# Kernel optimization log

Measured on AMD Instinct MI355X. Metric: run time of the kernel, lower is better.

Reference implementation:

```python
import jax, jax.numpy as jnp
import numpy as np

# ---- problem dims ----
B, S, C, H, W = 4, 8, 3, 256, 256
P = 68          # keypoints (self.points)
DS = 4          # detector downsample
WIN = 8
STEPS = 10      # Gauss-Newton iterations per frame pair
EPS = 1e-6
GRAY_W = jnp.array([0.299, 0.587, 0.114], dtype=jnp.float32)

# window offsets [K,2] in (x,y)
_rng = jnp.arange(-WIN, WIN + 1, dtype=jnp.float32)
_OFF = jnp.stack(jnp.meshgrid(_rng, _rng, indexing='xy'), -1).reshape(-1, 2)


def setup_inputs() -> dict:
    key = jax.random.key(0)
    k1, k2 = jax.random.split(key)
    inputs = jax.random.normal(k1, (B, S, C, H, W), dtype=jnp.float32)
    Wdet = jax.random.normal(k2, (P, C, 3, 3), dtype=jnp.float32) * 0.1
    bdet = jnp.zeros((P,), dtype=jnp.float32)
    return {"inputs": inputs, "Wdet": Wdet, "bdet": bdet}


def _bilinear(img, xy):
    # img [H,W]; xy [...,2] in (x,y) pixel coords -> sampled values [...]
    x = jnp.clip(xy[..., 0], 0.0, W - 1.001)
    y = jnp.clip(xy[..., 1], 0.0, H - 1.001)
    x0 = jnp.floor(x); y0 = jnp.floor(y)
    wx = x - x0; wy = y - y0
    x0i = x0.astype(jnp.int32); y0i = y0.astype(jnp.int32)
    x1i = jnp.minimum(x0i + 1, W - 1); y1i = jnp.minimum(y0i + 1, H - 1)
    v00 = img[y0i, x0i]; v01 = img[y0i, x1i]
    v10 = img[y1i, x0i]; v11 = img[y1i, x1i]
    return (1 - wy) * ((1 - wx) * v00 + wx * v01) + wy * ((1 - wx) * v10 + wx * v11)


def _grad_xy(img):
    # central differences with edge replication
    px = jnp.pad(img, ((0, 0), (1, 1)), mode='edge')
    py = jnp.pad(img, ((1, 1), (0, 0)), mode='edge')
    gx = (px[:, 2:] - px[:, :-2]) * 0.5
    gy = (py[2:, :] - py[:-2, :]) * 0.5
    return gx, gy


def _lk_track(old, new, pts):
    # one Lucas-Kanade tracking step: old/new [H,W] gray, pts [P,2] -> [P,2]
    gx, gy = _grad_xy(old)
    pos0 = pts[:, None, :] + _OFF[None]            # [P,K,2]
    I0 = _bilinear(old, pos0)                      # [P,K] template patch
    Ix = _bilinear(gx, pos0)
    Iy = _bilinear(gy, pos0)
    Gxx = (Ix * Ix).sum(-1); Gxy = (Ix * Iy).sum(-1); Gyy = (Iy * Iy).sum(-1)
    det = Gxx * Gyy - Gxy * Gxy + EPS
    Ginv = jnp.stack([jnp.stack([Gyy, -Gxy], -1),
                      jnp.stack([-Gxy, Gxx], -1)], -2) / det[:, None, None]  # [P,2,2]

    def step(i, v):
        I1 = _bilinear(new, pos0 + v[:, None, :])  # [P,K]
        err = I0 - I1
        b = jnp.stack([(err * Ix).sum(-1), (err * Iy).sum(-1)], -1)  # [P,2]
        return v + jnp.einsum('pij,pj->pi', Ginv, b)

    v = jax.lax.fori_loop(0, STEPS, step, jnp.zeros_like(pts))
    return pts + v


def _lk_forward_backward(gray, locs):
    # gray [S,H,W], locs [S,P,2] -> nextPts, fbackPts, backPts each [S,P,2]
    def f(pts, frames):
        o, n = frames
        q = _lk_track(o, n, pts)
        return q, q

    # forward: track detector locs of frame 0 through the sequence
    _, fout = jax.lax.scan(f, locs[0], (gray[:-1], gray[1:]))
    nextPts = jnp.concatenate([locs[:1], fout], 0)
    ro, rn = gray[1:][::-1], gray[:-1][::-1]
    # forward-backward: track the forward end point back to frame 0
    _, fbout = jax.lax.scan(f, nextPts[-1], (ro, rn))
    fbackPts = jnp.concatenate([nextPts[-1:], fbout], 0)[::-1]
    # backward: track detector locs of last frame back through the sequence
    _, bout = jax.lax.scan(f, locs[-1], (ro, rn))
    backPts = jnp.concatenate([locs[-1:], bout], 0)[::-1]
    return nextPts, fbackPts, backPts


def _detector(x, Wdet, bdet):
    # x [N,C,H,W] -> heatmaps [N,P,H/DS,W/DS], locs [N,P,2] (pixel coords), scores [N,P]
    hm = jax.lax.conv_general_dilated(
        x, Wdet, window_strides=(DS, DS), padding='SAME',
        dimension_numbers=('NCHW', 'OIHW', 'NCHW')) + bdet[None, :, None, None]
    N, _, Hd, Wd = hm.shape
    flat = hm.reshape(N, P, Hd * Wd)
    prob = jax.nn.softmax(flat, axis=-1)
    ys, xs = jnp.meshgrid(jnp.arange(Hd, dtype=hm.dtype),
                          jnp.arange(Wd, dtype=hm.dtype), indexing='ij')
    ex = (prob * xs.reshape(-1)).sum(-1) * DS   # soft-argmax, upscaled to input px
    ey = (prob * ys.reshape(-1)).sum(-1) * DS
    locs = jnp.stack([ex, ey], -1)
    scos = flat.max(-1)
    return hm, locs, scos


def reference(inputs, Wdet, bdet):
    x = inputs.reshape(B * S, C, H, W)
    hm, locs, scos = _detector(x, Wdet, bdet)
    heatmaps = hm.reshape(B, S, P, H // DS, W // DS)
    batch_locs = locs.reshape(B, S, P, 2)
    batch_scos = scos.reshape(B, S, P)
    gray = jnp.einsum('bschw,c->bshw', inputs, GRAY_W)  # [B,S,H,W]
    nextPts, fbackPts, backPts = jax.vmap(_lk_forward_backward)(gray, batch_locs)
    return heatmaps, batch_locs, batch_scos, nextPts, fbackPts, backPts
```

## Files before the change

kernel.cpp:

```cpp
#include <hip/hip_runtime.h>
#include <math.h>

namespace {
constexpr int Bn = 4, Sn = 8, Cn = 3, Himg = 256, Wimg = 256;
constexpr int Pn = 68, DS = 4, WIN = 8, STEPS = 10;
constexpr int HWi = Himg * Wimg;
constexpr int NIMG = Bn * Sn;
constexpr int HD = Himg / DS, WD = Wimg / DS;
constexpr int Kwin = (2 * WIN + 1) * (2 * WIN + 1);
constexpr int P2ROWS = 257;
constexpr int P2FR = P2ROWS * 256;
constexpr int NSHIFT = NIMG * P2FR;
}

__global__ __launch_bounds__(256) void conv_kernel(const float* __restrict__ x,
                                                   const float* __restrict__ Wdet,
                                                   const float* __restrict__ bdet,
                                                   float* __restrict__ hm) {
    __shared__ float wsh[Pn * 27];
    __shared__ float bsh[Pn];
    __shared__ float insh[3][3][Wimg];
    int n = blockIdx.x >> 6;
    int oy = blockIdx.x & 63;
    int tid = threadIdx.x;
    for (int t = tid; t < Pn * 27; t += 256) wsh[t] = Wdet[t];
    if (tid < Pn) bsh[tid] = bdet[tid];
    for (int t = tid; t < 3 * 3 * Wimg; t += 256) {
        int c = t / (3 * Wimg);
        int r = (t / Wimg) % 3;
        int col = t % Wimg;
        insh[c][r][col] = x[(size_t)n * 3 * HWi + (size_t)c * HWi + (oy * 4 + r) * Wimg + col];
    }
    __syncthreads();
    int ox = tid & 63;
    int wid = tid >> 6;
    float in_reg[27];
    #pragma unroll
    for (int c = 0; c < 3; c++)
        #pragma unroll
        for (int ky = 0; ky < 3; ky++)
            #pragma unroll
            for (int kx = 0; kx < 3; kx++)
                in_reg[c * 9 + ky * 3 + kx] = insh[c][ky][ox * 4 + kx];
    #pragma unroll
    for (int i = 0; i < 17; i++) {
        int p = wid + i * 4;
        const float* w = &wsh[p * 27];
        float acc = bsh[p];
        #pragma unroll
        for (int j = 0; j < 27; j++) acc += w[j] * in_reg[j];
        hm[(size_t)n * Pn * 4096 + (size_t)p * 4096 + oy * 64 + ox] = acc;
    }
}

__global__ __launch_bounds__(256) void smax_kernel(const float* __restrict__ hm,
                                                   float* __restrict__ locs,
                                                   float* __restrict__ scos) {
    int row = blockIdx.x;
    const float4* r = (const float4*)(hm + (size_t)row * 4096);
    int tid = threadIdx.x;
    float v[16];
    #pragma unroll
    for (int j = 0; j < 4; j++) {
        float4 q = r[tid + 256 * j];
        v[4 * j + 0] = q.x; v[4 * j + 1] = q.y; v[4 * j + 2] = q.z; v[4 * j + 3] = q.w;
    }
    float m = v[0];
    #pragma unroll
    for (int i = 1; i < 16; i++) m = fmaxf(m, v[i]);
    __shared__ float redm[4];
    #pragma unroll
    for (int o = 32; o; o >>= 1) m = fmaxf(m, __shfl_xor(m, o, 64));
    int wid = tid >> 6, lane = tid & 63;
    if (lane == 0) redm[wid] = m;
    __syncthreads();
    m = fmaxf(fmaxf(redm[0], redm[1]), fmaxf(redm[2], redm[3]));
    float s = 0.f, sx = 0.f, sy = 0.f;
    #pragma unroll
    for (int j = 0; j < 4; j++) {
        #pragma unroll
        for (int q = 0; q < 4; q++) {
            int e = (tid + 256 * j) * 4 + q;
            float ev = expf(v[4 * j + q] - m);
            s += ev;
            sx += ev * (float)(e & 63);
            sy += ev * (float)(e >> 6);
        }
    }
    #pragma unroll
    for (int o = 32; o; o >>= 1) {
        s  += __shfl_xor(s, o, 64);
        sx += __shfl_xor(sx, o, 64);
        sy += __shfl_xor(sy, o, 64);
    }
    __shared__ float reds[3][4];
    if (lane == 0) { reds[0][wid] = s; reds[1][wid] = sx; reds[2][wid] = sy; }
    __syncthreads();
    if (tid == 0) {
        float S_ = reds[0][0] + reds[0][1] + reds[0][2] + reds[0][3];
        float SX = reds[1][0] + reds[1][1] + reds[1][2] + reds[1][3];
        float SY = reds[2][0] + reds[2][1] + reds[2][2] + reds[2][3];
        locs[(size_t)row * 2 + 0] = SX / S_ * 4.0f;
        locs[(size_t)row * 2 + 1] = SY / S_ * 4.0f;
        scos[row] = m;
    }
}

__global__ __launch_bounds__(256) void grayP2_kernel(const float* __restrict__ in,
                                                     float2* __restrict__ P2r,
                                                     float2* __restrict__ P2rs) {
    __shared__ float g[9][257];
    int blk = blockIdx.x;
    int n = blk / 33, q = blk % 33;
    int tid = threadIdx.x;
    const float* base = in + (size_t)n * 3 * HWi;
    #pragma unroll
    for (int r = 0; r < 9; r++) {
        int row = min(max(8 * q - 1 + r, 0), 255);
        int a = row * Wimg + tid;
        g[r][tid] = 0.299f * base[a] + 0.587f * base[a + HWi] + 0.114f * base[a + 2 * HWi];
    }
    if (tid < 9) g[tid][256] = g[tid][255];
    __syncthreads();
    float2* pr = P2r + (size_t)n * P2FR;
    float2* ps = P2rs + (size_t)n * P2FR;
    #pragma unroll
    for (int j = 0; j < 8; j++) {
        int k = 8 * q + j;
        if (k <= 256) {
            float a = g[j][tid], b = g[j + 1][tid];
            pr[k * 256 + tid] = make_float2(a, b);
            float a2 = g[j][tid + 1], b2 = g[j + 1][tid + 1];
            ps[k * 256 + tid] = make_float2(a2, b2);
        }
    }
}

template <int CTRL>
__device__ inline float dpp_add(float v) {
    int t = __builtin_amdgcn_update_dpp(0, __builtin_bit_cast(int, v), CTRL, 0xF, 0xF, true);
    return v + __builtin_bit_cast(float, t);
}

__device__ inline float wredw(float v) {
    v = dpp_add<0x111>(v);
    v = dpp_add<0x112>(v);
    v = dpp_add<0x114>(v);
    v = dpp_add<0x118>(v);
    v = dpp_add<0x142>(v);
    v = dpp_add<0x143>(v);
    int s = __builtin_amdgcn_readlane(__builtin_bit_cast(int, v), 63);
    return __builtin_bit_cast(float, s);
}

__device__ void lk_track_p2(const float2* __restrict__ Po, const float2* __restrict__ Pn,
                            float& px, float& py, const float* dxs, const float* dys,
                            float s4w) {
    const float XM = (float)(Wimg - 1.001);
    const float YM = (float)(Himg - 1.001);
    float I0[5], Ix[5], Iy[5], qx[5], qy[5];
    {
        float wx[5], wy[5];
        int idx[5], sb[5], xm[5], xp[5];
        #pragma unroll
        for (int j = 0; j < 5; j++) {
            qx[j] = px + dxs[j];
            qy[j] = py + dys[j];
            float x = fminf(fmaxf(qx[j], 0.0f), XM);
            float y = fminf(fmaxf(qy[j], 0.0f), YM);
            float xf = floorf(x), yf = floorf(y);
            wx[j] = x - xf; wy[j] = y - yf;
            int xi = (int)xf, yi = (int)yf;
            int col = xi & ~1;
            idx[j] = yi * 256 + col + ((xi & 1) ? NSHIFT : 0);
            sb[j] = (yi + 1) * 256;
            xm[j] = max(xi - 1, 0);
            xp[j] = min(xi + 2, Wimg - 1);
        }
        float4 A[5], B[5];
        float2 S1[5], S2[5];
        #pragma unroll
        for (int j = 0; j < 5; j++) {
            A[j] = *reinterpret_cast<const float4*>(Po + idx[j]);
            B[j] = *reinterpret_cast<const float4*>(Po + idx[j] + 512);
            S1[j] = Po[sb[j] + xm[j]];
            S2[j] = Po[sb[j] + xp[j]];
        }
        #pragma unroll
        for (int j = 0; j < 5; j++) {
            float m0 = A[j].x, c00 = A[j].y, m1 = A[j].z, c01 = A[j].w;
            float c10 = B[j].x, p0 = B[j].y, c11 = B[j].z, p1 = B[j].w;
            float c0m = S1[j].x, c1m = S1[j].y, c0p = S2[j].x, c1p = S2[j].y;
            float u = 1.0f - wx[j], t = 1.0f - wy[j];
            I0[j] = t * (u * c00 + wx[j] * c01) + wy[j] * (u * c10 + wx[j] * c11);
            float gx00 = 0.5f * (c01 - c0m);
            float gx01 = 0.5f * (c0p - c00);
            float gx10 = 0.5f * (c11 - c1m);
            float gx11 = 0.5f * (c1p - c10);
            Ix[j] = t * (u * gx00 + wx[j] * gx01) + wy[j] * (u * gx10 + wx[j] * gx11);
            float gy00 = 0.5f * (c10 - m0);
            float gy01 = 0.5f * (c11 - m1);
            float gy10 = 0.5f * (p0 - c00);
            float gy11 = 0.5f * (p1 - c01);
            Iy[j] = t * (u * gy00 + wx[j] * gy01) + wy[j] * (u * gy10 + wx[j] * gy11);
        }
        Ix[4] *= s4w;
        Iy[4] *= s4w;
    }
    float gxx = 0.f, gxy = 0.f, gyy = 0.f;
    #pragma unroll
    for (int j = 0; j < 5; j++) { gxx += Ix[j] * Ix[j]; gxy += Ix[j] * Iy[j]; gyy += Iy[j] * Iy[j]; }
    gxx = wredw(gxx); gxy = wredw(gxy); gyy = wredw(gyy);
    float det = gxx * gyy - gxy * gxy + 1e-6f;
    float A = gyy / det, Bv = -gxy / det, D = gxx / det;
    float vx = 0.f, vy = 0.f;
    for (int it = 0; it < STEPS; ++it) {
        float fx[5], fy[5];
        int id[5];
        #pragma unroll
        for (int j = 0; j < 5; j++) {
            float x = fminf(fmaxf(qx[j] + vx, 0.0f), XM);
            float y = fminf(fmaxf(qy[j] + vy, 0.0f), YM);
            float xf = floorf(x), yf = floorf(y);
            fx[j] = x - xf; fy[j] = y - yf;
            int xi = (int)xf, yi = (int)yf;
            id[j] = (yi + 1) * 256 + (xi & ~1) + ((xi & 1) ? NSHIFT : 0);
        }
        float4 Q[5];
        #pragma unroll
        for (int j = 0; j < 5; j++) Q[j] = *reinterpret_cast<const float4*>(Pn + id[j]);
        float bx = 0.f, by = 0.f;
        #pragma unroll
        for (int j = 0; j < 5; j++) {
            float u = 1.0f - fx[j], t = 1.0f - fy[j];
            float I1 = t * (u * Q[j].x + fx[j] * Q[j].z) + fy[j] * (u * Q[j].y + fx[j] * Q[j].w);
            float err = I0[j] - I1;
            bx += err * Ix[j];
            by += err * Iy[j];
        }
        bx = wredw(bx); by = wredw(by);
        vx += A * bx + Bv * by;
        vy += Bv * bx + D * by;
    }
    px += vx; py += vy;
}

__global__ __launch_bounds__(64) void lk_p2_kernel(const float2* __restrict__ P2r,
                                                   const float* __restrict__ locs,
                                                   float* __restrict__ nextPts,
                                                   float* __restrict__ fbackPts,
                                                   float* __restrict__ backPts) {
    int g = blockIdx.x;
    int typ = g / (Bn * Pn);
    int r = g % (Bn * Pn);
    int b = r / Pn;
    int p = r % Pn;
    int lane = threadIdx.x;
    const float2* F = P2r + (size_t)b * Sn * P2FR;
    float dxs[5], dys[5];
    #pragma unroll
    for (int j = 0; j < 4; j++) {
        int k = lane + 64 * j;
        dxs[j] = (float)(k % 17 - 8);
        dys[j] = (float)(k / 17 - 8);
    }
    {
        int k4 = (lane < Kwin - 256) ? 256 + lane : 256;
        dxs[4] = (float)(k4 % 17 - 8);
        dys[4] = (float)(k4 / 17 - 8);
    }
    float s4w = (lane < Kwin - 256) ? 1.0f : 0.0f;
    auto LIDX = [&](int s) { return (((size_t)b * Sn + s) * Pn + p) * 2; };
    if (typ == 0) {
        float px = locs[LIDX(0)], py = locs[LIDX(0) + 1];
        if (lane == 0) { nextPts[LIDX(0)] = px; nextPts[LIDX(0) + 1] = py; }
        for (int s = 0; s < 7; s++) {
            lk_track_p2(F + s * P2FR, F + (s + 1) * P2FR, px, py, dxs, dys, s4w);
            if (lane == 0) { nextPts[LIDX(s + 1)] = px; nextPts[LIDX(s + 1) + 1] = py; }
        }
        if (lane == 0) { fbackPts[LIDX(7)] = px; fbackPts[LIDX(7) + 1] = py; }
        for (int i = 0; i < 7; i++) {
            lk_track_p2(F + (7 - i) * P2FR, F + (6 - i) * P2FR, px, py, dxs, dys, s4w);
            if (lane == 0) { fbackPts[LIDX(6 - i)] = px; fbackPts[LIDX(6 - i) + 1] = py; }
        }
    } else {
        float px = locs[LIDX(7)], py = locs[LIDX(7) + 1];
        if (lane == 0) { backPts[LIDX(7)] = px; backPts[LIDX(7) + 1] = py; }
        for (int i = 0; i < 7; i++) {
            lk_track_p2(F + (7 - i) * P2FR, F + (6 - i) * P2FR, px, py, dxs, dys, s4w);
            if (lane == 0) { backPts[LIDX(6 - i)] = px; backPts[LIDX(6 - i) + 1] = py; }
        }
    }
}

__global__ __launch_bounds__(256) void gray2_kernel(const float* __restrict__ in,
                                                    float* __restrict__ gray,
                                                    float* __restrict__ sh) {
    int idx = blockIdx.x * blockDim.x + threadIdx.x;
    int total = NIMG * HWi / 4;
    if (idx >= total) return;
    int img = idx / (HWi / 4);
    int off = idx % (HWi / 4);
    const float* base = in + (size_t)img * 3 * HWi;
    float4 c0 = ((const float4*)(base))[off];
    float4 c1 = ((const float4*)(base + HWi))[off];
    float4 c2 = ((const float4*)(base + 2 * HWi))[off];
    float4 g;
    g.x = 0.299f * c0.x + 0.587f * c1.x + 0.114f * c2.x;
    g.y = 0.299f * c0.y + 0.587f * c1.y + 0.114f * c2.y;
    g.z = 0.299f * c0.z + 0.587f * c1.z + 0.114f * c2.z;
    g.w = 0.299f * c0.w + 0.587f * c1.w + 0.114f * c2.w;
    float gn = 0.f;
    int gi = idx * 4 + 4;
    if (gi < NIMG * HWi) {
        int i2 = gi / HWi;
        int o2 = gi % HWi;
        const float* b2 = in + (size_t)i2 * 3 * HWi;
        gn = 0.299f * b2[o2] + 0.587f * b2[o2 + HWi] + 0.114f * b2[o2 + 2 * HWi];
    }
    ((float4*)(gray + (size_t)img * HWi))[off] = g;
    float4 s;
    s.x = g.y; s.y = g.z; s.z = g.w; s.w = gn;
    ((float4*)(sh + (size_t)img * HWi))[off] = s;
}

__device__ void lk_track_pair(const float* __restrict__ oldI, const float* __restrict__ oldS,
                              const float* __restrict__ newI, const float* __restrict__ newS,
                              float& px, float& py, const float* dxs, const float* dys,
                              float s4w) {
    const float XM = (float)(Wimg - 1.001);
    const float YM = (float)(Himg - 1.001);
    float I0[5], Ix[5], Iy[5], qx[5], qy[5];
    {
        float wx[5], wy[5];
        const float* pb[5];
        int xe[5], am[5], a0[5], a1[5], ap[5], xm[5], xp[5];
        #pragma unroll
        for (int j = 0; j < 5; j++) {
            qx[j] = px + dxs[j];
            qy[j] = py + dys[j];
            float x = fminf(fmaxf(qx[j], 0.0f), XM);
            float y = fminf(fmaxf(qy[j], 0.0f), YM);
            float x0f = floorf(x), y0f = floorf(y);
            wx[j] = x - x0f; wy[j] = y - y0f;
            int xi = (int)x0f, yi = (int)y0f;
            xe[j] = xi & ~1;
            pb[j] = (xi & 1) ? oldS : oldI;
            xm[j] = max(xi - 1, 0);
            xp[j] = min(xi + 2, Wimg - 1);
            a0[j] = yi * Wimg;
            a1[j] = a0[j] + Wimg;
            am[j] = max(yi - 1, 0) * Wimg;
            ap[j] = min(yi + 2, Himg - 1) * Wimg;
        }
        float2 Pm[5], P0[5], P1[5], Pp[5];
        float c0m[5], c0p[5], c1m[5], c1p[5];
        #pragma unroll
        for (int j = 0; j < 5; j++) {
            Pm[j] = *(const float2*)(pb[j] + am[j] + xe[j]);
            P0[j] = *(const float2*)(pb[j] + a0[j] + xe[j]);
            P1[j] = *(const float2*)(pb[j] + a1[j] + xe[j]);
            Pp[j] = *(const float2*)(pb[j] + ap[j] + xe[j]);
            c0m[j] = oldI[a0[j] + xm[j]];
            c0p[j] = oldI[a0[j] + xp[j]];
            c1m[j] = oldI[a1[j] + xm[j]];
            c1p[j] = oldI[a1[j] + xp[j]];
        }
        #pragma unroll
        for (int j = 0; j < 5; j++) {
            float m0 = Pm[j].x, m1 = Pm[j].y;
            float c00 = P0[j].x, c01 = P0[j].y;
            float c10 = P1[j].x, c11 = P1[j].y;
            float p0 = Pp[j].x, p1 = Pp[j].y;
            float u = 1.0f - wx[j], t = 1.0f - wy[j];
            I0[j] = t * (u * c00 + wx[j] * c01) + wy[j] * (u * c10 + wx[j] * c11);
            float gx00 = 0.5f * (c01 - c0m[j]);
            float gx01 = 0.5f * (c0p[j] - c00);
            float gx10 = 0.5f * (c11 - c1m[j]);
            float gx11 = 0.5f * (c1p[j] - c10);
            Ix[j] = t * (u * gx00 + wx[j] * gx01) + wy[j] * (u * gx10 + wx[j] * gx11);
            float gy00 = 0.5f * (c10 - m0);
            float gy01 = 0.5f * (c11 - m1);
            float gy10 = 0.5f * (p0 - c00);
            float gy11 = 0.5f * (p1 - c01);
            Iy[j] = t * (u * gy00 + wx[j] * gy01) + wy[j] * (u * gy10 + wx[j] * gy11);
        }
        Ix[4] *= s4w;
        Iy[4] *= s4w;
    }
    float gxx = 0.f, gxy = 0.f, gyy = 0.f;
    #pragma unroll
    for (int j = 0; j < 5; j++) { gxx += Ix[j] * Ix[j]; gxy += Ix[j] * Iy[j]; gyy += Iy[j] * Iy[j]; }
    gxx = wredw(gxx); gxy = wredw(gxy); gyy = wredw(gyy);
    float det = gxx * gyy - gxy * gxy + 1e-6f;
    float A = gyy / det, Bv = -gxy / det, D = gxx / det;
    float vx = 0.f, vy = 0.f;
    for (int it = 0; it < STEPS; ++it) {
        float fx[5], fy[5];
        const float* pb[5];
        int aa[5];
        #pragma unroll
        for (int j = 0; j < 5; j++) {
            float x = fminf(fmaxf(qx[j] + vx, 0.0f), XM);
            float y = fminf(fmaxf(qy[j] + vy, 0.0f), YM);
            float x0f = floorf(x), y0f = floorf(y);
            fx[j] = x - x0f; fy[j] = y - y0f;
            int xi = (int)x0f, yi = (int)y0f;
            pb[j] = (xi & 1) ? newS : newI;
            aa[j] = yi * Wimg + (xi & ~1);
        }
        float2 R0[5], R1[5];
        #pragma unroll
        for (int j = 0; j < 5; j++) {
            R0[j] = *(const float2*)(pb[j] + aa[j]);
            R1[j] = *(const float2*)(pb[j] + aa[j] + Wimg);
        }
        float bx = 0.f, by = 0.f;
        #pragma unroll
        for (int j = 0; j < 5; j++) {
            float u = 1.0f - fx[j], t = 1.0f - fy[j];
            float I1 = t * (u * R0[j].x + fx[j] * R0[j].y) + fy[j] * (u * R1[j].x + fx[j] * R1[j].y);
            float err = I0[j] - I1;
            bx += err * Ix[j];
            by += err * Iy[j];
        }
        bx = wredw(bx); by = wredw(by);
        vx += A * bx + Bv * by;
        vy += Bv * bx + D * by;
    }
    px += vx; py += vy;
}

__global__ __launch_bounds__(64) void lk_pair_kernel(const float* __restrict__ gray,
                                                     const float* __restrict__ sh,
                                                     const float* __restrict__ locs,
                                                     float* __restrict__ nextPts,
                                                     float* __restrict__ fbackPts,
                                                     float* __restrict__ backPts) {
    int g = blockIdx.x;
    int typ = g / (Bn * Pn);
    int r = g % (Bn * Pn);
    int b = r / Pn;
    int p = r % Pn;
    int lane = threadIdx.x;
    const float* G = gray + (size_t)b * Sn * HWi;
    const float* S = sh + (size_t)b * Sn * HWi;
    float dxs[5], dys[5];
    #pragma unroll
    for (int j = 0; j < 4; j++) {
        int k = lane + 64 * j;
        dxs[j] = (float)(k % 17 - 8);
        dys[j] = (float)(k / 17 - 8);
    }
    {
        int k4 = (lane < Kwin - 256) ? 256 + lane : 256;
        dxs[4] = (float)(k4 % 17 - 8);
        dys[4] = (float)(k4 / 17 - 8);
    }
    float s4w = (lane < Kwin - 256) ? 1.0f : 0.0f;
    auto LIDX = [&](int s) { return (((size_t)b * Sn + s) * Pn + p) * 2; };
    if (typ == 0) {
        float px = locs[LIDX(0)], py = locs[LIDX(0) + 1];
        if (lane == 0) { nextPts[LIDX(0)] = px; nextPts[LIDX(0) + 1] = py; }
        for (int s = 0; s < 7; s++) {
            lk_track_pair(G + s * HWi, S + s * HWi, G + (s + 1) * HWi, S + (s + 1) * HWi,
                          px, py, dxs, dys, s4w);
            if (lane == 0) { nextPts[LIDX(s + 1)] = px; nextPts[LIDX(s + 1) + 1] = py; }
        }
        if (lane == 0) { fbackPts[LIDX(7)] = px; fbackPts[LIDX(7) + 1] = py; }
        for (int i = 0; i < 7; i++) {
            lk_track_pair(G + (7 - i) * HWi, S + (7 - i) * HWi, G + (6 - i) * HWi, S + (6 - i) * HWi,
                          px, py, dxs, dys, s4w);
            if (lane == 0) { fbackPts[LIDX(6 - i)] = px; fbackPts[LIDX(6 - i) + 1] = py; }
        }
    } else {
        float px = locs[LIDX(7)], py = locs[LIDX(7) + 1];
        if (lane == 0) { backPts[LIDX(7)] = px; backPts[LIDX(7) + 1] = py; }
        for (int i = 0; i < 7; i++) {
            lk_track_pair(G + (7 - i) * HWi, S + (7 - i) * HWi, G + (6 - i) * HWi, S + (6 - i) * HWi,
                          px, py, dxs, dys, s4w);
            if (lane == 0) { backPts[LIDX(6 - i)] = px; backPts[LIDX(6 - i) + 1] = py; }
        }
    }
}

__device__ inline float px_fly(const float* __restrict__ im, int idx) {
    return 0.299f * im[idx] + 0.587f * im[idx + HWi] + 0.114f * im[idx + 2 * HWi];
}

__device__ void lk_track_fly(const float* __restrict__ oldI, const float* __restrict__ newI,
                             float& px, float& py, const float* dxs, const float* dys,
                             float s4w) {
    const float XM = (float)(Wimg - 1.001);
    const float YM = (float)(Himg - 1.001);
    float I0[5], Ix[5], Iy[5], qx[5], qy[5];
    {
        float wx[5], wy[5];
        int am[5], a0[5], a1[5], ap[5], xm[5], x0[5], x1[5], xp[5];
        #pragma unroll
        for (int j = 0; j < 5; j++) {
            qx[j] = px + dxs[j]; qy[j] = py + dys[j];
            float x = fminf(fmaxf(qx[j], 0.0f), XM);
            float y = fminf(fmaxf(qy[j], 0.0f), YM);
            float x0f = floorf(x), y0f = floorf(y);
            wx[j] = x - x0f; wy[j] = y - y0f;
            int xi = (int)x0f, yi = (int)y0f;
            x0[j] = xi; x1[j] = min(xi + 1, Wimg - 1);
            xm[j] = max(xi - 1, 0); xp[j] = min(xi + 2, Wimg - 1);
            a0[j] = yi * Wimg;
            a1[j] = min(yi + 1, Himg - 1) * Wimg;
            am[j] = max(yi - 1, 0) * Wimg;
            ap[j] = min(yi + 2, Himg - 1) * Wimg;
        }
        #pragma unroll
        for (int j = 0; j < 5; j++) {
            float m0 = px_fly(oldI, am[j] + x0[j]), m1 = px_fly(oldI, am[j] + x1[j]);
            float c0m = px_fly(oldI, a0[j] + xm[j]), c00 = px_fly(oldI, a0[j] + x0[j]);
            float c01 = px_fly(oldI, a0[j] + x1[j]), c0p = px_fly(oldI, a0[j] + xp[j]);
            float c1m = px_fly(oldI, a1[j] + xm[j]), c10 = px_fly(oldI, a1[j] + x0[j]);
            float c11 = px_fly(oldI, a1[j] + x1[j]), c1p = px_fly(oldI, a1[j] + xp[j]);
            float p0 = px_fly(oldI, ap[j] + x0[j]), p1 = px_fly(oldI, ap[j] + x1[j]);
            float u = 1.0f - wx[j], t = 1.0f - wy[j];
            I0[j] = t * (u * c00 + wx[j] * c01) + wy[j] * (u * c10 + wx[j] * c11);
            Ix[j] = t * (u * 0.5f * (c01 - c0m) + wx[j] * 0.5f * (c0p - c00))
                  + wy[j] * (u * 0.5f * (c11 - c1m) + wx[j] * 0.5f * (c1p - c10));
            Iy[j] = t * (u * 0.5f * (c10 - m0) + wx[j] * 0.5f * (c11 - m1))
                  + wy[j] * (u * 0.5f * (p0 - c00) + wx[j] * 0.5f * (p1 - c01));
        }
        Ix[4] *= s4w; Iy[4] *= s4w;
    }
    float gxx = 0.f, gxy = 0.f, gyy = 0.f;
    #pragma unroll
    for (int j = 0; j < 5; j++) { gxx += Ix[j] * Ix[j]; gxy += Ix[j] * Iy[j]; gyy += Iy[j] * Iy[j]; }
    gxx = wredw(gxx); gxy = wredw(gxy); gyy = wredw(gyy);
    float det = gxx * gyy - gxy * gxy + 1e-6f;
    float A = gyy / det, Bv = -gxy / det, D = gxx / det;
    float vx = 0.f, vy = 0.f;
    for (int it = 0; it < STEPS; ++it) {
        float bx = 0.f, by = 0.f;
        #pragma unroll
        for (int j = 0; j < 5; j++) {
            float x = fminf(fmaxf(qx[j] + vx, 0.0f), XM);
            float y = fminf(fmaxf(qy[j] + vy, 0.0f), YM);
            float x0f = floorf(x), y0f = floorf(y);
            float fxx = x - x0f, fyy = y - y0f;
            int xi = (int)x0f, yi = (int)y0f;
            int ad = yi * Wimg + xi;
            int d1 = (xi < Wimg - 1) ? 1 : 0;
            int d2 = (yi < Himg - 1) ? Wimg : 0;
            float v00 = px_fly(newI, ad), v01 = px_fly(newI, ad + d1);
            float v10 = px_fly(newI, ad + d2), v11 = px_fly(newI, ad + d2 + d1);
            float u = 1.0f - fxx, t = 1.0f - fyy;
            float I1 = t * (u * v00 + fxx * v01) + fyy * (u * v10 + fxx * v11);
            float err = I0[j] - I1;
            bx += err * Ix[j];
            by += err * Iy[j];
        }
        bx = wredw(bx); by = wredw(by);
        vx += A * bx + Bv * by;
        vy += Bv * bx + D * by;
    }
    px += vx; py += vy;
}

__global__ __launch_bounds__(64) void lk_fly_kernel(const float* __restrict__ in,
                                                    const float* __restrict__ locs,
                                                    float* __restrict__ nextPts,
                                                    float* __restrict__ fbackPts,
                                                    float* __restrict__ backPts) {
    constexpr size_t FS = (size_t)3 * HWi;
    int g = blockIdx.x;
    int typ = g / (Bn * Pn);
    int r = g % (Bn * Pn);
    int b = r / Pn;
    int p = r % Pn;
    int lane = threadIdx.x;
    const float* G = in + (size_t)b * Sn * FS;
    float dxs[5], dys[5];
    #pragma unroll
    for (int j = 0; j < 4; j++) {
        int k = lane + 64 * j;
        dxs[j] = (float)(k % 17 - 8);
        dys[j] = (float)(k / 17 - 8);
    }
    {
        int k4 = (lane < Kwin - 256) ? 256 + lane : 256;
        dxs[4] = (float)(k4 % 17 - 8);
        dys[4] = (float)(k4 / 17 - 8);
    }
    float s4w = (lane < Kwin - 256) ? 1.0f : 0.0f;
    auto LIDX = [&](int s) { return (((size_t)b * Sn + s) * Pn + p) * 2; };
    if (typ == 0) {
        float px = locs[LIDX(0)], py = locs[LIDX(0) + 1];
        if (lane == 0) { nextPts[LIDX(0)] = px; nextPts[LIDX(0) + 1] = py; }
        for (int s = 0; s < 7; s++) {
            lk_track_fly(G + s * FS, G + (s + 1) * FS, px, py, dxs, dys, s4w);
            if (lane == 0) { nextPts[LIDX(s + 1)] = px; nextPts[LIDX(s + 1) + 1] = py; }
        }
        if (lane == 0) { fbackPts[LIDX(7)] = px; fbackPts[LIDX(7) + 1] = py; }
        for (int i = 0; i < 7; i++) {
            lk_track_fly(G + (7 - i) * FS, G + (6 - i) * FS, px, py, dxs, dys, s4w);
            if (lane == 0) { fbackPts[LIDX(6 - i)] = px; fbackPts[LIDX(6 - i) + 1] = py; }
        }
    } else {
        float px = locs[LIDX(7)], py = locs[LIDX(7) + 1];
        if (lane == 0) { backPts[LIDX(7)] = px; backPts[LIDX(7) + 1] = py; }
        for (int i = 0; i < 7; i++) {
            lk_track_fly(G + (7 - i) * FS, G + (6 - i) * FS, px, py, dxs, dys, s4w);
            if (lane == 0) { backPts[LIDX(6 - i)] = px; backPts[LIDX(6 - i) + 1] = py; }
        }
    }
}

extern "C" void kernel_launch(void* const* d_in, const int* in_sizes, int n_in,
                              void* d_out, int out_size, void* d_ws, size_t ws_size,
                              hipStream_t stream) {
    const float* inputs = (const float*)d_in[0];
    const float* Wdet = (const float*)d_in[1];
    const float* bdet = (const float*)d_in[2];
    float* out = (float*)d_out;

    const size_t N_hm = (size_t)Bn * Sn * Pn * HD * WD;
    const size_t N_pts = (size_t)Bn * Sn * Pn * 2;
    float* hm = out;
    float* locs = out + N_hm;
    float* scos = locs + N_pts;
    float* nextPts = scos + (size_t)Bn * Sn * Pn;
    float* fbackPts = nextPts + N_pts;
    float* backPts = fbackPts + N_pts;

    conv_kernel<<<NIMG * 64, 256, 0, stream>>>(inputs, Wdet, bdet, hm);
    smax_kernel<<<NIMG * Pn, 256, 0, stream>>>(hm, locs, scos);

    const size_t p2_bytes = (size_t)2 * NIMG * P2FR * sizeof(float2);
    const size_t gray_elems = (size_t)NIMG * HWi;
    if (ws_size >= p2_bytes) {
        float2* P2r = (float2*)d_ws;
        float2* P2rs = P2r + (size_t)NIMG * P2FR;
        grayP2_kernel<<<NIMG * 33, 256, 0, stream>>>(inputs, P2r, P2rs);
        lk_p2_kernel<<<2 * Bn * Pn, 64, 0, stream>>>(P2r, locs, nextPts, fbackPts, backPts);
    } else if (ws_size >= 2 * gray_elems * sizeof(float)) {
        float* gray = (float*)d_ws;
        float* sh = gray + gray_elems;
        gray2_kernel<<<(NIMG * HWi / 4 + 255) / 256, 256, 0, stream>>>(inputs, gray, sh);
        lk_pair_kernel<<<2 * Bn * Pn, 64, 0, stream>>>(gray, sh, locs, nextPts, fbackPts, backPts);
    } else {
        lk_fly_kernel<<<2 * Bn * Pn, 64, 0, stream>>>(inputs, locs, nextPts, fbackPts, backPts);
    }
}
```

Baseline: 113.3 us.

## Fuse detector conv with gray pair-plane build and peel first LK iteration

Merges the strided detector convolution and the grayscale paired-row plane construction into one kernel. Each block loads five input rows once and uses them for both the heatmap and the gray planes, so the input is read once instead of twice and one launch is removed. In the LK tracker, the first Gauss-Newton iteration's new-image samples are now loaded together with the template loads, since the displacement is zero at that point. This overlaps that iteration's memory latency with template setup, at the cost of more registers and extra LDS in the fused kernel.

```diff
diff --git a/kernel.cpp b/kernel.cpp
--- a/kernel.cpp
+++ b/kernel.cpp
@@ -11,6 +11,68 @@
 constexpr int P2ROWS = 257;
 constexpr int P2FR = P2ROWS * 256;
 constexpr int NSHIFT = NIMG * P2FR;
+}
+
+__global__ __launch_bounds__(256) void mega_kernel(const float* __restrict__ x,
+                                                   const float* __restrict__ Wdet,
+                                                   const float* __restrict__ bdet,
+                                                   float* __restrict__ hm,
+                                                   float2* __restrict__ P2r,
+                                                   float2* __restrict__ P2rs) {
+    __shared__ float wsh[Pn * 27];
+    __shared__ float bsh[Pn];
+    __shared__ float insh[3][5][Wimg];
+    __shared__ float grow[5][257];
+    int n = blockIdx.x >> 6;
+    int oy = blockIdx.x & 63;
+    int tid = threadIdx.x;
+    for (int t = tid; t < Pn * 27; t += 256) wsh[t] = Wdet[t];
+    if (tid < Pn) bsh[tid] = bdet[tid];
+    for (int t = tid; t < 3 * 5 * Wimg; t += 256) {
+        int c = t / (5 * Wimg);
+        int rem = t % (5 * Wimg);
+        int r = rem / Wimg;
+        int col = rem % Wimg;
+        int gr = min(max(4 * oy - 1 + r, 0), 255);
+        insh[c][r][col] = x[(size_t)n * 3 * HWi + (size_t)c * HWi + gr * Wimg + col];
+    }
+    __syncthreads();
+    int ox = tid & 63;
+    int wid = tid >> 6;
+    float in_reg[27];
+    #pragma unroll
+    for (int c = 0; c < 3; c++)
+        #pragma unroll
+        for (int ky = 0; ky < 3; ky++)
+            #pragma unroll
+            for (int kx = 0; kx < 3; kx++)
+                in_reg[c * 9 + ky * 3 + kx] = insh[c][1 + ky][ox * 4 + kx];
+    #pragma unroll
+    for (int i = 0; i < 17; i++) {
+        int p = wid + i * 4;
+        const float* w = &wsh[p * 27];
+        float acc = bsh[p];
+        #pragma unroll
+        for (int j = 0; j < 27; j++) acc += w[j] * in_reg[j];
+        hm[(size_t)n * Pn * 4096 + (size_t)p * 4096 + oy * 64 + ox] = acc;
+    }
+    #pragma unroll
+    for (int r = 0; r < 5; r++)
+        grow[r][tid] = 0.299f * insh[0][r][tid] + 0.587f * insh[1][r][tid] + 0.114f * insh[2][r][tid];
+    if (tid < 5) grow[tid][256] = grow[tid][255];
+    __syncthreads();
+    float2* pr = P2r + (size_t)n * P2FR;
+    float2* ps = P2rs + (size_t)n * P2FR;
+    #pragma unroll
+    for (int j = 0; j < 4; j++) {
+        int k = 4 * oy + j;
+        pr[k * 256 + tid] = make_float2(grow[j][tid], grow[j + 1][tid]);
+        ps[k * 256 + tid] = make_float2(grow[j][tid + 1], grow[j + 1][tid + 1]);
+    }
+    if (oy == 63) {
+        pr[256 * 256 + tid] = make_float2(grow[4][tid], grow[4][tid]);
+        ps[256 * 256 + tid] = make_float2(grow[4][tid + 1], grow[4][tid + 1]);
+    }
 }
 
 __global__ __launch_bounds__(256) void conv_kernel(const float* __restrict__ x,
@@ -106,36 +168,6 @@
     }
 }
 
-__global__ __launch_bounds__(256) void grayP2_kernel(const float* __restrict__ in,
-                                                     float2* __restrict__ P2r,
-                                                     float2* __restrict__ P2rs) {
-    __shared__ float g[9][257];
-    int blk = blockIdx.x;
-    int n = blk / 33, q = blk % 33;
-    int tid = threadIdx.x;
-    const float* base = in + (size_t)n * 3 * HWi;
-    #pragma unroll
-    for (int r = 0; r < 9; r++) {
-        int row = min(max(8 * q - 1 + r, 0), 255);
-        int a = row * Wimg + tid;
-        g[r][tid] = 0.299f * base[a] + 0.587f * base[a + HWi] + 0.114f * base[a + 2 * HWi];
-    }
-    if (tid < 9) g[tid][256] = g[tid][255];
-    __syncthreads();
-    float2* pr = P2r + (size_t)n * P2FR;
-    float2* ps = P2rs + (size_t)n * P2FR;
-    #pragma unroll
-    for (int j = 0; j < 8; j++) {
-        int k = 8 * q + j;
-        if (k <= 256) {
-            float a = g[j][tid], b = g[j + 1][tid];
-            pr[k * 256 + tid] = make_float2(a, b);
-            float a2 = g[j][tid + 1], b2 = g[j + 1][tid + 1];
-            ps[k * 256 + tid] = make_float2(a2, b2);
-        }
-    }
-}
-
 template <int CTRL>
 __device__ inline float dpp_add(float v) {
     int t = __builtin_amdgcn_update_dpp(0, __builtin_bit_cast(int, v), CTRL, 0xF, 0xF, true);
@@ -159,9 +191,10 @@
     const float XM = (float)(Wimg - 1.001);
     const float YM = (float)(Himg - 1.001);
     float I0[5], Ix[5], Iy[5], qx[5], qy[5];
+    float wx[5], wy[5];
+    float4 Q0[5];
     {
-        float wx[5], wy[5];
-        int idx[5], sb[5], xm[5], xp[5];
+        int idx[5], sb[5], xm[5], xp[5], id0[5];
         #pragma unroll
         for (int j = 0; j < 5; j++) {
             qx[j] = px + dxs[j];
@@ -172,8 +205,10 @@
             wx[j] = x - xf; wy[j] = y - yf;
             int xi = (int)xf, yi = (int)yf;
             int col = xi & ~1;
-            idx[j] = yi * 256 + col + ((xi & 1) ? NSHIFT : 0);
+            int sel = (xi & 1) ? NSHIFT : 0;
+            idx[j] = yi * 256 + col + sel;
             sb[j] = (yi + 1) * 256;
+            id0[j] = sb[j] + col + sel;
             xm[j] = max(xi - 1, 0);
             xp[j] = min(xi + 2, Wimg - 1);
         }
@@ -185,6 +220,7 @@
             B[j] = *reinterpret_cast<const float4*>(Po + idx[j] + 512);
             S1[j] = Po[sb[j] + xm[j]];
             S2[j] = Po[sb[j] + xp[j]];
+            Q0[j] = *reinterpret_cast<const float4*>(Pn + id0[j]);
         }
         #pragma unroll
         for (int j = 0; j < 5; j++) {
@@ -214,7 +250,21 @@
     float det = gxx * gyy - gxy * gxy + 1e-6f;
     float A = gyy / det, Bv = -gxy / det, D = gxx / det;
     float vx = 0.f, vy = 0.f;
-    for (int it = 0; it < STEPS; ++it) {
+    {
+        float bx = 0.f, by = 0.f;
+        #pragma unroll
+        for (int j = 0; j < 5; j++) {
+            float u = 1.0f - wx[j], t = 1.0f - wy[j];
+            float I1 = t * (u * Q0[j].x + wx[j] * Q0[j].z) + wy[j] * (u * Q0[j].y + wx[j] * Q0[j].w);
+            float err = I0[j] - I1;
+            bx += err * Ix[j];
+            by += err * Iy[j];
+        }
+        bx = wredw(bx); by = wredw(by);
+        vx += A * bx + Bv * by;
+        vy += Bv * bx + D * by;
+    }
+    for (int it = 1; it < STEPS; ++it) {
         float fx[5], fy[5];
         int id[5];
         #pragma unroll
@@ -629,22 +679,24 @@
     float* fbackPts = nextPts + N_pts;
     float* backPts = fbackPts + N_pts;
 
-    conv_kernel<<<NIMG * 64, 256, 0, stream>>>(inputs, Wdet, bdet, hm);
-    smax_kernel<<<NIMG * Pn, 256, 0, stream>>>(hm, locs, scos);
-
     const size_t p2_bytes = (size_t)2 * NIMG * P2FR * sizeof(float2);
     const size_t gray_elems = (size_t)NIMG * HWi;
     if (ws_size >= p2_bytes) {
         float2* P2r = (float2*)d_ws;
         float2* P2rs = P2r + (size_t)NIMG * P2FR;
-        grayP2_kernel<<<NIMG * 33, 256, 0, stream>>>(inputs, P2r, P2rs);
+        mega_kernel<<<NIMG * 64, 256, 0, stream>>>(inputs, Wdet, bdet, hm, P2r, P2rs);
+        smax_kernel<<<NIMG * Pn, 256, 0, stream>>>(hm, locs, scos);
         lk_p2_kernel<<<2 * Bn * Pn, 64, 0, stream>>>(P2r, locs, nextPts, fbackPts, backPts);
     } else if (ws_size >= 2 * gray_elems * sizeof(float)) {
+        conv_kernel<<<NIMG * 64, 256, 0, stream>>>(inputs, Wdet, bdet, hm);
+        smax_kernel<<<NIMG * Pn, 256, 0, stream>>>(hm, locs, scos);
         float* gray = (float*)d_ws;
         float* sh = gray + gray_elems;
         gray2_kernel<<<(NIMG * HWi / 4 + 255) / 256, 256, 0, stream>>>(inputs, gray, sh);
         lk_pair_kernel<<<2 * Bn * Pn, 64, 0, stream>>>(gray, sh, locs, nextPts, fbackPts, backPts);
     } else {
+        conv_kernel<<<NIMG * 64, 256, 0, stream>>>(inputs, Wdet, bdet, hm);
+        smax_kernel<<<NIMG * Pn, 256, 0, stream>>>(hm, locs, scos);
         lk_fly_kernel<<<2 * Bn * Pn, 64, 0, stream>>>(inputs, locs, nextPts, fbackPts, backPts);
     }
 }
```

After: 112.0 us. No clear change (-1.1%).
